# Performance work log

Measured on AMD Instinct MI355X. Metric: run time of the kernel, lower is better.

The kernel has to match this reference:

```python
import jax, jax.numpy as jnp
import numpy as np

WS = 7          # window_size (square)
HEADS = 12


def _relative_position_index(ws=WS):
    # Faithful port of WindowAttentionBase._get_relative_position_index
    coords = np.stack(np.meshgrid(np.arange(ws), np.arange(ws), indexing='ij'))  # [2, ws, ws]
    flat = coords.reshape(2, -1)                       # [2, n]
    rel = flat[:, :, None] - flat[:, None, :]          # [2, n, n]
    rel = rel.transpose(1, 2, 0)                       # [n, n, 2]
    rel[:, :, 0] += ws - 1
    rel[:, :, 1] += ws - 1
    rel[:, :, 0] *= 2 * ws - 1
    return jnp.asarray(rel.sum(-1).reshape(-1), dtype=jnp.int32)  # [n*n]


def setup_inputs() -> dict:
    key = jax.random.key(0)
    ks = jax.random.split(key, 6)
    b, H, W, c = 32, 56, 56, 384
    return {
        "x": jax.random.normal(ks[0], (b, H, W, c), jnp.float32),
        "w_qkv": jax.random.normal(ks[1], (3 * c, c), jnp.float32) * (c ** -0.5),
        "b_qkv": jax.random.normal(ks[2], (3 * c,), jnp.float32) * 0.02,
        "rel_pos": jax.random.normal(ks[3], (HEADS, (2 * WS - 1) ** 2), jnp.float32),
        "w_out": jax.random.normal(ks[4], (c, c), jnp.float32) * (c ** -0.5),
        "b_out": jax.random.normal(ks[5], (c,), jnp.float32) * 0.02,
    }


def reference(x, w_qkv, b_qkv, rel_pos, w_out, b_out):
    b, H, W, c = x.shape
    g = HEADS
    d = c // g
    hn, wn = H // WS, W // WS
    n = WS * WS
    scale = d ** -0.5

    # split_into_windows: 'b (p h) (q w) c -> b h w (p q) c'  (p,q = window dims, OUTER factors)
    xw = x.reshape(b, WS, hn, WS, wn, c).transpose(0, 2, 4, 1, 3, 5).reshape(b, hn, wn, n, c)

    qkv = xw @ w_qkv.T + b_qkv                          # [b, hn, wn, n, 3c]
    q, k, v = jnp.split(qkv, 3, axis=-1)
    # 'b h w n (g d) -> b g h w n d'
    to_heads = lambda t: t.reshape(b, hn, wn, n, g, d).transpose(0, 4, 1, 2, 3, 5)
    q, k, v = to_heads(q) * scale, to_heads(k), to_heads(v)

    sim = jnp.einsum('bghwnd,bghwmd->bghwnm', q, k)     # [b, g, hn, wn, n, n]
    idx = _relative_position_index()
    bias = rel_pos[:, idx].reshape(g, n, n)             # gather relative position bias
    sim = sim + bias[None, :, None, None, :, :]

    attn = jax.nn.softmax(sim, axis=-1)
    out = jnp.einsum('bghwnm,bghwmd->bghwnd', attn, v)  # [b, g, hn, wn, n, d]

    # 'b g h w n d -> b h w n (g d)' then merge_windows 'b h w (p q) c -> b (p h) (q w) c'
    out = out.transpose(0, 2, 3, 4, 1, 5).reshape(b, hn, wn, n, c)
    out = out.reshape(b, hn, wn, WS, WS, c).transpose(0, 3, 1, 4, 2, 5).reshape(b, H, W, c)
    return out @ w_out.T + b_out
```

## Files before the change

kernel.cpp:

```cpp
#include <hip/hip_runtime.h>

typedef __attribute__((ext_vector_type(8))) short bf16x8;
typedef __attribute__((ext_vector_type(4))) float f32x4;

__device__ __forceinline__ unsigned short f2bf(float f){
  unsigned u = __builtin_bit_cast(unsigned, f);
  u += 0x7fffu + ((u >> 16) & 1u);
  return (unsigned short)(u >> 16);
}

__device__ __forceinline__ unsigned cvt_pk_bf16(float lo, float hi){
  unsigned r;
  asm("v_cvt_pk_bf16_f32 %0, %1, %2" : "=v"(r) : "v"(lo), "v"(hi));
  return r;
}

#define ASYNC16(ldsp, gp) __builtin_amdgcn_global_load_lds( \
    (const __attribute__((address_space(1))) unsigned int*)(gp), \
    (__attribute__((address_space(3))) unsigned int*)(ldsp), 16, 0, 0)

__global__ __launch_bounds__(256) void convert_x_kernel(const float* __restrict__ x,
                                                        unsigned short* __restrict__ xb){
  int idx = blockIdx.x*256 + threadIdx.x;
  int token = idx / 96, j = idx - token*96;
  int b = token / 3136, rem = token - b*3136;
  int rr = rem / 56, cp = rem - rr*56;
  int p = rr >> 3, h = rr & 7, q = cp >> 3, w = cp & 7;
  int orow = ((b*8 + h)*8 + w)*49 + p*7 + q;
  float4 v = *(const float4*)(x + (size_t)idx*4);
  ushort4 o;
  o.x = f2bf(v.x); o.y = f2bf(v.y); o.z = f2bf(v.z); o.w = f2bf(v.w);
  *(ushort4*)(xb + (size_t)orow*384 + j*4) = o;
}

__global__ __launch_bounds__(256) void convert_w_kernel(const float* __restrict__ wq,
                                                        const float* __restrict__ wo,
                                                        unsigned short* __restrict__ wqb,
                                                        unsigned short* __restrict__ wob){
  int idx = blockIdx.x*256 + threadIdx.x;
  if (idx < 110592){
    float4 v = *(const float4*)(wq + (size_t)idx*4);
    ushort4 o; o.x=f2bf(v.x); o.y=f2bf(v.y); o.z=f2bf(v.z); o.w=f2bf(v.w);
    *(ushort4*)(wqb + (size_t)idx*4) = o;
  } else {
    int k = idx - 110592;
    float4 v = *(const float4*)(wo + (size_t)k*4);
    ushort4 o; o.x=f2bf(v.x); o.y=f2bf(v.y); o.z=f2bf(v.z); o.w=f2bf(v.w);
    *(ushort4*)(wob + (size_t)k*4) = o;
  }
}

__global__ __launch_bounds__(256) void build_btab(const float* __restrict__ rel_pos,
                                                  float* __restrict__ btab){
  int idx = blockIdx.x*256 + threadIdx.x;
  int head = idx >> 10, rem = idx & 1023;
  int fi = rem >> 6, lane = rem & 63;
  int ti = fi >> 2, tj = fi & 3;
  int qq = tj*16 + (lane & 15);
  int kb = ti*16 + (lane >> 4)*4;
  float4 v; float* vp = (float*)&v;
#pragma unroll
  for (int r=0; r<4; ++r){
    int kk = kb + r;
    float val;
    if (kk >= 49) val = -__builtin_inff();
    else if (qq >= 49) val = 0.f;
    else {
      int ip = qq/7, iq = qq - ip*7, jp = kk/7, jq = kk - jp*7;
      val = rel_pos[head*169 + (ip-jp+6)*13 + (iq-jq+6)] * 1.4426950408889634f;
    }
    vp[r] = val;
  }
  *(float4*)(btab + (size_t)idx*4) = v;
}

template<int EPI, int NBY>
__global__ __launch_bounds__(256) void gemm128(const unsigned short* __restrict__ A,
                                               const unsigned short* __restrict__ B,
                                               const float* __restrict__ bias,
                                               unsigned short* __restrict__ qo,
                                               unsigned short* __restrict__ ko,
                                               unsigned short* __restrict__ vo,
                                               float* __restrict__ out)
{
  constexpr int K = 384;
  constexpr int NT = 12;
  __shared__ unsigned short Al[3][128*32];
  __shared__ unsigned short Bl[3][128*32];
  const int tid = threadIdx.x;
  const int lane = tid & 63, wid = tid >> 6;
  const int wr = wid >> 1, wc = wid & 1;
  const int l15 = lane & 15, kg = lane >> 4;
  const int swz = (l15 >> 1) & 3;
  const int cswz = (tid & 3) ^ ((tid >> 3) & 3);

  const int n = blockIdx.x;
  const int xcd = n & 7, s = n >> 3;
  const int panel = s / NBY, nb = s - panel*NBY;
  const int bx = panel*8 + xcd, by = nb;

  const unsigned short* Ag = A + ((size_t)bx*128 + (tid>>2))*K + cswz*8;
  const unsigned short* Bg = B + ((size_t)by*128 + (tid>>2))*K + cswz*8;

  f32x4 acc[4][4] = {};

#define STAGE(buf, kt) do { \
    ASYNC16(&Al[buf][wid*512],        Ag + (kt)*32); \
    ASYNC16(&Al[buf][wid*512 + 2048], Ag + (size_t)64*K + (kt)*32); \
    ASYNC16(&Bl[buf][wid*512],        Bg + (kt)*32); \
    ASYNC16(&Bl[buf][wid*512 + 2048], Bg + (size_t)64*K + (kt)*32); \
  } while(0)

  STAGE(0,0); STAGE(1,1);

#pragma unroll
  for (int t = 0; t < NT; ++t){
    if (t < NT-1) asm volatile("s_waitcnt vmcnt(4)\n\ts_barrier" ::: "memory");
    else          asm volatile("s_waitcnt vmcnt(0)\n\ts_barrier" ::: "memory");

    if (t + 2 < NT) STAGE((t+2)%3, t+2);

    const unsigned short* Ab = Al[t % 3];
    const unsigned short* Bb = Bl[t % 3];
    bf16x8 af[4], bfv[4];
#pragma unroll
    for (int ti=0; ti<4; ++ti)
      af[ti] = *(const bf16x8*)(Ab + (wr*64 + ti*16 + l15)*32 + (kg ^ swz)*8);
#pragma unroll
    for (int tj=0; tj<4; ++tj)
      bfv[tj] = *(const bf16x8*)(Bb + (wc*64 + tj*16 + l15)*32 + (kg ^ swz)*8);

    __builtin_amdgcn_s_setprio(1);
#pragma unroll
    for (int ti=0; ti<4; ++ti)
#pragma unroll
      for (int tj=0; tj<4; ++tj)
        acc[ti][tj] = __builtin_amdgcn_mfma_f32_16x16x32_bf16(af[ti], bfv[tj], acc[ti][tj], 0,0,0);
    __builtin_amdgcn_s_setprio(0);
  }
#undef STAGE

  const int rbase = bx*128 + wr*64 + kg*4;

  if (EPI == 0){
    const int t = by / 3;
    unsigned short* __restrict__ Pout = (t==0) ? qo : ((t==1) ? ko : vo);
    const float scale = (t==0) ? (0.17677669529663689f * 1.4426950408889634f) : 1.0f;
    const int cb = (by - t*3)*128 + wc*64;
    int hoff[4]; float bvs[4];
#pragma unroll
    for (int tj=0; tj<4; ++tj){
      int colt = cb + tj*16;
      hoff[tj] = (colt>>5)*1568 + (colt&31) + l15;
      bvs[tj] = bias[by*128 + wc*64 + tj*16 + l15] * scale;
    }
#pragma unroll
    for (int ti=0; ti<4; ++ti){
#pragma unroll
      for (int r=0; r<4; ++r){
        int R = rbase + ti*16 + r;
        int win = R / 49, nn = R - win*49;
        size_t rowoff = (size_t)win*18816 + nn*32;
#pragma unroll
        for (int tj=0; tj<4; ++tj)
          Pout[rowoff + hoff[tj]] = f2bf(acc[ti][tj][r]*scale + bvs[tj]);
      }
    }
  } else {
    const int cbs = by*128 + wc*64;
    float bv[4];
#pragma unroll
    for (int tj=0; tj<4; ++tj) bv[tj] = bias[cbs + tj*16 + l15];
#pragma unroll
    for (int ti=0; ti<4; ++ti){
#pragma unroll
      for (int r=0; r<4; ++r){
        int R = rbase + ti*16 + r;
        int win = R / 49, nn = R - win*49;
        int p = nn / 7, q = nn - p*7;
        int h = (win >> 3) & 7, w = win & 7;
        size_t tok = (size_t)(win >> 6)*3136 + (size_t)((p*8 + h)*56 + q*8 + w);
        float* __restrict__ orow = out + tok*384 + cbs + l15;
#pragma unroll
        for (int tj=0; tj<4; ++tj)
          orow[tj*16] = acc[ti][tj][r] + bv[tj];
      }
    }
  }
}

__global__ __launch_bounds__(256) void attn_kernel(const unsigned short* __restrict__ q,
                                                   const unsigned short* __restrict__ k,
                                                   const unsigned short* __restrict__ v,
                                                   const float* __restrict__ btab,
                                                   unsigned short* __restrict__ ao)
{
  __shared__ unsigned short P[4][4096];
  const int tid = threadIdx.x, lane = tid & 63, wid = tid >> 6;
  const int l15 = lane & 15, kg = lane >> 4;
  const int win = blockIdx.x / 3;
  const int head = (blockIdx.x % 3)*4 + wid;
  const size_t base = ((size_t)win*12 + head)*1568;
  const unsigned short* qb = q + base;
  const unsigned short* kb = k + base;
  const unsigned short* vb = v + base;
  const float* bt = btab + head*4096;

  bf16x8 vfk[2][2];
#pragma unroll
  for (int ks=0; ks<2; ++ks)
#pragma unroll
    for (int tjv=0; tjv<2; ++tjv)
#pragma unroll
      for (int e=0; e<8; ++e)
        vfk[ks][tjv][e] = (short)vb[(ks*32 + kg*8 + e)*32 + tjv*16 + l15];

  f32x4 s[4][4];
#pragma unroll
  for (int ti=0; ti<4; ++ti)
#pragma unroll
    for (int tj=0; tj<4; ++tj)
      s[ti][tj] = *(const f32x4*)(bt + ((ti*4 + tj)*64 + lane)*4);

  bf16x8 kf[4], qf[4];
#pragma unroll
  for (int ti=0; ti<4; ++ti) kf[ti] = *(const bf16x8*)(kb + (ti*16+l15)*32 + kg*8);
#pragma unroll
  for (int tj=0; tj<4; ++tj) qf[tj] = *(const bf16x8*)(qb + (tj*16+l15)*32 + kg*8);

  __builtin_amdgcn_s_setprio(1);
#pragma unroll
  for (int ti=0; ti<4; ++ti)
#pragma unroll
    for (int tj=0; tj<4; ++tj)
      s[ti][tj] = __builtin_amdgcn_mfma_f32_16x16x32_bf16(kf[ti], qf[tj], s[ti][tj], 0,0,0);
  __builtin_amdgcn_s_setprio(0);

  float rinv[4];
#pragma unroll
  for (int tj=0; tj<4; ++tj){
    float sum = 0.f;
#pragma unroll
    for (int ti=0; ti<4; ++ti)
#pragma unroll
      for (int r=0; r<4; ++r){
        float e = exp2f(s[ti][tj][r]);
        s[ti][tj][r] = e;
        sum += e;
      }
    sum += __shfl_xor(sum, 16);
    sum += __shfl_xor(sum, 32);
    rinv[tj] = __builtin_amdgcn_rcpf(sum);
  }

  unsigned short* Pl = P[wid];
  const unsigned swz = (unsigned)((l15 & 7) << 4);
#pragma unroll
  for (int tj=0; tj<4; ++tj){
    const float rv = rinv[tj];
    const unsigned rowb = (unsigned)((tj*16 + l15)*128);
#pragma unroll
    for (int ti=0; ti<4; ++ti){
      uint2 d;
      d.x = cvt_pk_bf16(s[ti][tj][0]*rv, s[ti][tj][1]*rv);
      d.y = cvt_pk_bf16(s[ti][tj][2]*rv, s[ti][tj][3]*rv);
      unsigned boff = (rowb + (unsigned)(ti*32 + kg*8)) ^ swz;
      *(uint2*)((char*)Pl + boff) = d;
    }
  }

  f32x4 o[4][2] = {};
#pragma unroll
  for (int oti=0; oti<4; ++oti){
    bf16x8 pa[2];
#pragma unroll
    for (int ks=0; ks<2; ++ks){
      unsigned boff = ((unsigned)((oti*16+l15)*128 + ks*64 + kg*16)) ^ swz;
      pa[ks] = *(const bf16x8*)((char*)Pl + boff);
    }
    __builtin_amdgcn_s_setprio(1);
#pragma unroll
    for (int tjv=0; tjv<2; ++tjv){
      o[oti][tjv] = __builtin_amdgcn_mfma_f32_16x16x32_bf16(pa[0], vfk[0][tjv], o[oti][tjv], 0,0,0);
      o[oti][tjv] = __builtin_amdgcn_mfma_f32_16x16x32_bf16(pa[1], vfk[1][tjv], o[oti][tjv], 0,0,0);
    }
    __builtin_amdgcn_s_setprio(0);
  }

#pragma unroll
  for (int oti=0; oti<4; ++oti)
#pragma unroll
    for (int r=0; r<4; ++r){
      int row = oti*16 + kg*4 + r;
      if (row < 49){
        unsigned short* op = ao + ((size_t)win*49 + row)*384 + head*32 + l15;
        op[0]  = (unsigned short)cvt_pk_bf16(o[oti][0][r], o[oti][0][r]);
        op[16] = (unsigned short)cvt_pk_bf16(o[oti][1][r], o[oti][1][r]);
      }
    }
}

extern "C" void kernel_launch(void* const* d_in, const int* in_sizes, int n_in,
                              void* d_out, int out_size, void* d_ws, size_t ws_size,
                              hipStream_t stream)
{
  const float* x       = (const float*)d_in[0];
  const float* w_qkv   = (const float*)d_in[1];
  const float* b_qkv   = (const float*)d_in[2];
  const float* rel_pos = (const float*)d_in[3];
  const float* w_out   = (const float*)d_in[4];
  const float* b_out   = (const float*)d_in[5];
  float* out = (float*)d_out;

  char* ws = (char*)d_ws;
  unsigned short* wqb = (unsigned short*)ws;
  unsigned short* wob = (unsigned short*)(ws + 884736);
  float* btab         = (float*)(ws + 884736 + 294912);
  unsigned short* qws = (unsigned short*)(ws + 1376256);
  unsigned short* kws = qws + 38535168;
  unsigned short* vws = kws + 38535168;
  unsigned short* xb  = vws + 38535168;
  unsigned short* ao  = xb;

  convert_x_kernel<<<dim3(37632), dim3(256), 0, stream>>>(x, xb);
  convert_w_kernel<<<dim3(576),   dim3(256), 0, stream>>>(w_qkv, w_out, wqb, wob);
  build_btab<<<dim3(48), dim3(256), 0, stream>>>(rel_pos, btab);
  gemm128<0,9><<<dim3(7056), dim3(256), 0, stream>>>(xb, wqb, b_qkv, qws, kws, vws, nullptr);
  attn_kernel<<<dim3(6144), dim3(256), 0, stream>>>(qws, kws, vws, btab, ao);
  gemm128<1,3><<<dim3(2352), dim3(256), 0, stream>>>(ao, wob, b_out, nullptr, nullptr, nullptr, out);
}
```

Measured before the change: 309.6 us.

## Load GEMM B operand directly from global into registers, bypassing LDS

The weight (B) tiles in the bf16 GEMM are no longer staged through shared memory. Each wave loads its own B fragments straight from global memory into a double-buffered register array, while A stays on the triple-buffered LDS async path. This halves LDS footprint and LDS read traffic per tile, which can raise occupancy. In exchange, the two column-half waves sharing a B slice each fetch it separately, and the loads are uncoalesced row-strided 16-byte accesses. The waitcnt counts are adjusted to cover the extra outstanding register loads.

After: 403.9 us. +30.4%, slower.

```diff
diff --git a/kernel.cpp b/kernel.cpp
--- a/kernel.cpp
+++ b/kernel.cpp
@@ -86,7 +86,6 @@
   constexpr int K = 384;
   constexpr int NT = 12;
   __shared__ unsigned short Al[3][128*32];
-  __shared__ unsigned short Bl[3][128*32];
   const int tid = threadIdx.x;
   const int lane = tid & 63, wid = tid >> 6;
   const int wr = wid >> 1, wc = wid & 1;
@@ -100,45 +99,52 @@
   const int bx = panel*8 + xcd, by = nb;
 
   const unsigned short* Ag = A + ((size_t)bx*128 + (tid>>2))*K + cswz*8;
-  const unsigned short* Bg = B + ((size_t)by*128 + (tid>>2))*K + cswz*8;
+  const unsigned short* Bg0 = B + ((size_t)(by*128 + wc*64 + l15))*K + kg*8;
+  const unsigned short* Bg1 = Bg0 + (size_t)16*K;
+  const unsigned short* Bg2 = Bg0 + (size_t)32*K;
+  const unsigned short* Bg3 = Bg0 + (size_t)48*K;
 
   f32x4 acc[4][4] = {};
-
-#define STAGE(buf, kt) do { \
+  bf16x8 bfr[2][4];
+
+#define STAGE_A(buf, kt) do { \
     ASYNC16(&Al[buf][wid*512],        Ag + (kt)*32); \
     ASYNC16(&Al[buf][wid*512 + 2048], Ag + (size_t)64*K + (kt)*32); \
-    ASYNC16(&Bl[buf][wid*512],        Bg + (kt)*32); \
-    ASYNC16(&Bl[buf][wid*512 + 2048], Bg + (size_t)64*K + (kt)*32); \
   } while(0)
-
-  STAGE(0,0); STAGE(1,1);
+#define LOADB(d, kt) do { \
+    bfr[d][0] = *(const bf16x8*)(Bg0 + (kt)*32); \
+    bfr[d][1] = *(const bf16x8*)(Bg1 + (kt)*32); \
+    bfr[d][2] = *(const bf16x8*)(Bg2 + (kt)*32); \
+    bfr[d][3] = *(const bf16x8*)(Bg3 + (kt)*32); \
+  } while(0)
+
+  STAGE_A(0,0); STAGE_A(1,1);
+  LOADB(0, 0);
 
 #pragma unroll
   for (int t = 0; t < NT; ++t){
-    if (t < NT-1) asm volatile("s_waitcnt vmcnt(4)\n\ts_barrier" ::: "memory");
-    else          asm volatile("s_waitcnt vmcnt(0)\n\ts_barrier" ::: "memory");
-
-    if (t + 2 < NT) STAGE((t+2)%3, t+2);
+    if (t < NT-1) asm volatile("s_waitcnt vmcnt(6)\n\ts_barrier" ::: "memory");
+    else          asm volatile("s_waitcnt vmcnt(4)\n\ts_barrier" ::: "memory");
+
+    if (t + 2 < NT) STAGE_A((t+2)%3, t+2);
+    if (t + 1 < NT) LOADB((t+1)&1, t+1);
 
     const unsigned short* Ab = Al[t % 3];
-    const unsigned short* Bb = Bl[t % 3];
-    bf16x8 af[4], bfv[4];
+    bf16x8 af[4];
 #pragma unroll
     for (int ti=0; ti<4; ++ti)
       af[ti] = *(const bf16x8*)(Ab + (wr*64 + ti*16 + l15)*32 + (kg ^ swz)*8);
-#pragma unroll
-    for (int tj=0; tj<4; ++tj)
-      bfv[tj] = *(const bf16x8*)(Bb + (wc*64 + tj*16 + l15)*32 + (kg ^ swz)*8);
 
     __builtin_amdgcn_s_setprio(1);
 #pragma unroll
     for (int ti=0; ti<4; ++ti)
 #pragma unroll
       for (int tj=0; tj<4; ++tj)
-        acc[ti][tj] = __builtin_amdgcn_mfma_f32_16x16x32_bf16(af[ti], bfv[tj], acc[ti][tj], 0,0,0);
+        acc[ti][tj] = __builtin_amdgcn_mfma_f32_16x16x32_bf16(af[ti], bfr[t&1][tj], acc[ti][tj], 0,0,0);
     __builtin_amdgcn_s_setprio(0);
   }
-#undef STAGE
+#undef STAGE_A
+#undef LOADB
 
   const int rbase = bx*128 + wr*64 + kg*4;
 
```

## Fuse x fp32-to-bf16 window conversion into the QKV GEMM A-tile loads

Applied to the files above, without the earlier changes.

Removes the standalone convert_x kernel. The QKV GEMM now gathers fp32 x rows directly by window token index, converts them to bf16 in registers and writes them swizzled into a double-buffered LDS A tile. The weight tile keeps its async global-to-LDS path with triple buffering. This avoids a full write and re-read of the bf16 windowed copy of x, but each block now reads fp32 A data, twice the bytes, repeated across the nine N tiles, and carries more register pressure.

After: 348.7 us. +12.6%, slower.

```diff
diff --git a/kernel.cpp b/kernel.cpp
--- a/kernel.cpp
+++ b/kernel.cpp
@@ -18,20 +18,6 @@
 #define ASYNC16(ldsp, gp) __builtin_amdgcn_global_load_lds( \
     (const __attribute__((address_space(1))) unsigned int*)(gp), \
     (__attribute__((address_space(3))) unsigned int*)(ldsp), 16, 0, 0)
-
-__global__ __launch_bounds__(256) void convert_x_kernel(const float* __restrict__ x,
-                                                        unsigned short* __restrict__ xb){
-  int idx = blockIdx.x*256 + threadIdx.x;
-  int token = idx / 96, j = idx - token*96;
-  int b = token / 3136, rem = token - b*3136;
-  int rr = rem / 56, cp = rem - rr*56;
-  int p = rr >> 3, h = rr & 7, q = cp >> 3, w = cp & 7;
-  int orow = ((b*8 + h)*8 + w)*49 + p*7 + q;
-  float4 v = *(const float4*)(x + (size_t)idx*4);
-  ushort4 o;
-  o.x = f2bf(v.x); o.y = f2bf(v.y); o.z = f2bf(v.z); o.w = f2bf(v.w);
-  *(ushort4*)(xb + (size_t)orow*384 + j*4) = o;
-}
 
 __global__ __launch_bounds__(256) void convert_w_kernel(const float* __restrict__ wq,
                                                         const float* __restrict__ wo,
@@ -74,14 +60,131 @@
   *(float4*)(btab + (size_t)idx*4) = v;
 }
 
-template<int EPI, int NBY>
-__global__ __launch_bounds__(256) void gemm128(const unsigned short* __restrict__ A,
-                                               const unsigned short* __restrict__ B,
-                                               const float* __restrict__ bias,
-                                               unsigned short* __restrict__ qo,
-                                               unsigned short* __restrict__ ko,
-                                               unsigned short* __restrict__ vo,
-                                               float* __restrict__ out)
+__global__ __launch_bounds__(256) void gemm_qkv(const float* __restrict__ X,
+                                                const unsigned short* __restrict__ B,
+                                                const float* __restrict__ bias,
+                                                unsigned short* __restrict__ qo,
+                                                unsigned short* __restrict__ ko,
+                                                unsigned short* __restrict__ vo)
+{
+  constexpr int K = 384;
+  constexpr int NT = 12;
+  __shared__ unsigned short Al[2][4096];
+  __shared__ unsigned short Bl[3][4096];
+  const int tid = threadIdx.x;
+  const int lane = tid & 63, wid = tid >> 6;
+  const int wr = wid >> 1, wc = wid & 1;
+  const int l15 = lane & 15, kg = lane >> 4;
+  const int swz = (l15 >> 1) & 3;
+  const int cswz = (tid & 3) ^ ((tid >> 3) & 3);
+
+  const int n = blockIdx.x;
+  const int xcd = n & 7, s = n >> 3;
+  const int panel = s / 9, nb = s - panel*9;
+  const int bx = panel*8 + xcd, by = nb;
+
+  const int r1 = tid >> 2, c4 = tid & 3;
+  int R1 = bx*128 + r1, R2 = R1 + 64;
+  int win1 = R1/49, nn1 = R1 - win1*49, p1 = nn1/7, q1 = nn1 - p1*7;
+  int win2 = R2/49, nn2 = R2 - win2*49, p2 = nn2/7, q2 = nn2 - p2*7;
+  size_t tok1 = (size_t)(win1>>6)*3136 + (p1*8 + ((win1>>3)&7))*56 + q1*8 + (win1&7);
+  size_t tok2 = (size_t)(win2>>6)*3136 + (p2*8 + ((win2>>3)&7))*56 + q2*8 + (win2&7);
+  const float* Xg1 = X + tok1*384 + c4*8;
+  const float* Xg2 = X + tok2*384 + c4*8;
+  const int wch = (c4 ^ ((r1 >> 1) & 3)) * 8;
+  unsigned short* Aw1base = &Al[0][0] + r1*32 + wch;
+  unsigned short* Aw2base = Aw1base + 64*32;
+
+  const unsigned short* Bg = B + ((size_t)(by*128 + (tid>>2)))*K + cswz*8;
+
+  f32x4 acc[4][4] = {};
+  float4 aA0[2], aA1[2], aB0[2], aB1[2];
+
+#define LOADA(st, kt) do { \
+    aA0[st] = *(const float4*)(Xg1 + (kt)*32); \
+    aA1[st] = *(const float4*)(Xg1 + (kt)*32 + 4); \
+    aB0[st] = *(const float4*)(Xg2 + (kt)*32); \
+    aB1[st] = *(const float4*)(Xg2 + (kt)*32 + 4); \
+  } while(0)
+#define WRITEA(st, buf) do { \
+    uint4 u1, u2; \
+    u1.x = cvt_pk_bf16(aA0[st].x, aA0[st].y); u1.y = cvt_pk_bf16(aA0[st].z, aA0[st].w); \
+    u1.z = cvt_pk_bf16(aA1[st].x, aA1[st].y); u1.w = cvt_pk_bf16(aA1[st].z, aA1[st].w); \
+    u2.x = cvt_pk_bf16(aB0[st].x, aB0[st].y); u2.y = cvt_pk_bf16(aB0[st].z, aB0[st].w); \
+    u2.z = cvt_pk_bf16(aB1[st].x, aB1[st].y); u2.w = cvt_pk_bf16(aB1[st].z, aB1[st].w); \
+    *(uint4*)(Aw1base + (buf)*4096) = u1; \
+    *(uint4*)(Aw2base + (buf)*4096) = u2; \
+  } while(0)
+#define STAGE_B(buf, kt) do { \
+    ASYNC16(&Bl[buf][wid*512],        Bg + (kt)*32); \
+    ASYNC16(&Bl[buf][wid*512 + 2048], Bg + (size_t)64*K + (kt)*32); \
+  } while(0)
+
+  LOADA(0, 0); STAGE_B(0, 0);
+  LOADA(1, 1); STAGE_B(1, 1);
+  asm volatile("s_waitcnt vmcnt(8)" ::: "memory");
+  WRITEA(0, 0);
+
+#pragma unroll
+  for (int t = 0; t < NT; ++t){
+    if (t < NT-1) asm volatile("s_waitcnt vmcnt(6) lgkmcnt(0)\n\ts_barrier" ::: "memory");
+    else          asm volatile("s_waitcnt vmcnt(0) lgkmcnt(0)\n\ts_barrier" ::: "memory");
+
+    if (t < NT-1) WRITEA((t+1)&1, (t+1)&1);
+    if (t < NT-2){ LOADA(t&1, t+2); STAGE_B((t+2)%3, t+2); }
+
+    const unsigned short* Ab = Al[t & 1];
+    const unsigned short* Bb = Bl[t % 3];
+    bf16x8 af[4], bfv[4];
+#pragma unroll
+    for (int ti=0; ti<4; ++ti)
+      af[ti] = *(const bf16x8*)(Ab + (wr*64 + ti*16 + l15)*32 + (kg ^ swz)*8);
+#pragma unroll
+    for (int tj=0; tj<4; ++tj)
+      bfv[tj] = *(const bf16x8*)(Bb + (wc*64 + tj*16 + l15)*32 + (kg ^ swz)*8);
+
+    __builtin_amdgcn_s_setprio(1);
+#pragma unroll
+    for (int ti=0; ti<4; ++ti)
+#pragma unroll
+      for (int tj=0; tj<4; ++tj)
+        acc[ti][tj] = __builtin_amdgcn_mfma_f32_16x16x32_bf16(af[ti], bfv[tj], acc[ti][tj], 0,0,0);
+    __builtin_amdgcn_s_setprio(0);
+  }
+#undef LOADA
+#undef WRITEA
+#undef STAGE_B
+
+  const int rbase = bx*128 + wr*64 + kg*4;
+  const int t = by / 3;
+  unsigned short* __restrict__ Pout = (t==0) ? qo : ((t==1) ? ko : vo);
+  const float scale = (t==0) ? (0.17677669529663689f * 1.4426950408889634f) : 1.0f;
+  const int cb = (by - t*3)*128 + wc*64;
+  int hoff[4]; float bvs[4];
+#pragma unroll
+  for (int tj=0; tj<4; ++tj){
+    int colt = cb + tj*16;
+    hoff[tj] = (colt>>5)*1568 + (colt&31) + l15;
+    bvs[tj] = bias[by*128 + wc*64 + tj*16 + l15] * scale;
+  }
+#pragma unroll
+  for (int ti=0; ti<4; ++ti){
+#pragma unroll
+    for (int r=0; r<4; ++r){
+      int R = rbase + ti*16 + r;
+      int win = R / 49, nn = R - win*49;
+      size_t rowoff = (size_t)win*18816 + nn*32;
+#pragma unroll
+      for (int tj=0; tj<4; ++tj)
+        Pout[rowoff + hoff[tj]] = f2bf(acc[ti][tj][r]*scale + bvs[tj]);
+    }
+  }
+}
+
+__global__ __launch_bounds__(256) void gemm_out(const unsigned short* __restrict__ A,
+                                                const unsigned short* __restrict__ B,
+                                                const float* __restrict__ bias,
+                                                float* __restrict__ out)
 {
   constexpr int K = 384;
   constexpr int NT = 12;
@@ -96,11 +199,11 @@
 
   const int n = blockIdx.x;
   const int xcd = n & 7, s = n >> 3;
-  const int panel = s / NBY, nb = s - panel*NBY;
+  const int panel = s / 3, nb = s - panel*3;
   const int bx = panel*8 + xcd, by = nb;
 
   const unsigned short* Ag = A + ((size_t)bx*128 + (tid>>2))*K + cswz*8;
-  const unsigned short* Bg = B + ((size_t)by*128 + (tid>>2))*K + cswz*8;
+  const unsigned short* Bg = B + ((size_t)(by*128 + (tid>>2)))*K + cswz*8;
 
   f32x4 acc[4][4] = {};
 
@@ -141,50 +244,23 @@
 #undef STAGE
 
   const int rbase = bx*128 + wr*64 + kg*4;
-
-  if (EPI == 0){
-    const int t = by / 3;
-    unsigned short* __restrict__ Pout = (t==0) ? qo : ((t==1) ? ko : vo);
-    const float scale = (t==0) ? (0.17677669529663689f * 1.4426950408889634f) : 1.0f;
-    const int cb = (by - t*3)*128 + wc*64;
-    int hoff[4]; float bvs[4];
-#pragma unroll
-    for (int tj=0; tj<4; ++tj){
-      int colt = cb + tj*16;
-      hoff[tj] = (colt>>5)*1568 + (colt&31) + l15;
-      bvs[tj] = bias[by*128 + wc*64 + tj*16 + l15] * scale;
-    }
-#pragma unroll
-    for (int ti=0; ti<4; ++ti){
-#pragma unroll
-      for (int r=0; r<4; ++r){
-        int R = rbase + ti*16 + r;
-        int win = R / 49, nn = R - win*49;
-        size_t rowoff = (size_t)win*18816 + nn*32;
-#pragma unroll
-        for (int tj=0; tj<4; ++tj)
-          Pout[rowoff + hoff[tj]] = f2bf(acc[ti][tj][r]*scale + bvs[tj]);
-      }
-    }
-  } else {
-    const int cbs = by*128 + wc*64;
-    float bv[4];
-#pragma unroll
-    for (int tj=0; tj<4; ++tj) bv[tj] = bias[cbs + tj*16 + l15];
-#pragma unroll
-    for (int ti=0; ti<4; ++ti){
-#pragma unroll
-      for (int r=0; r<4; ++r){
-        int R = rbase + ti*16 + r;
-        int win = R / 49, nn = R - win*49;
-        int p = nn / 7, q = nn - p*7;
-        int h = (win >> 3) & 7, w = win & 7;
-        size_t tok = (size_t)(win >> 6)*3136 + (size_t)((p*8 + h)*56 + q*8 + w);
-        float* __restrict__ orow = out + tok*384 + cbs + l15;
-#pragma unroll
-        for (int tj=0; tj<4; ++tj)
-          orow[tj*16] = acc[ti][tj][r] + bv[tj];
-      }
+  const int cbs = by*128 + wc*64;
+  float bv[4];
+#pragma unroll
+  for (int tj=0; tj<4; ++tj) bv[tj] = bias[cbs + tj*16 + l15];
+#pragma unroll
+  for (int ti=0; ti<4; ++ti){
+#pragma unroll
+    for (int r=0; r<4; ++r){
+      int R = rbase + ti*16 + r;
+      int win = R / 49, nn = R - win*49;
+      int p = nn / 7, q = nn - p*7;
+      int h = (win >> 3) & 7, w = win & 7;
+      size_t tok = (size_t)(win >> 6)*3136 + (size_t)((p*8 + h)*56 + q*8 + w);
+      float* __restrict__ orow = out + tok*384 + cbs + l15;
+#pragma unroll
+      for (int tj=0; tj<4; ++tj)
+        orow[tj*16] = acc[ti][tj][r] + bv[tj];
     }
   }
 }
@@ -319,13 +395,11 @@
   unsigned short* qws = (unsigned short*)(ws + 1376256);
   unsigned short* kws = qws + 38535168;
   unsigned short* vws = kws + 38535168;
-  unsigned short* xb  = vws + 38535168;
-  unsigned short* ao  = xb;
-
-  convert_x_kernel<<<dim3(37632), dim3(256), 0, stream>>>(x, xb);
-  convert_w_kernel<<<dim3(576),   dim3(256), 0, stream>>>(w_qkv, w_out, wqb, wob);
+  unsigned short* ao  = vws + 38535168;
+
+  convert_w_kernel<<<dim3(576), dim3(256), 0, stream>>>(w_qkv, w_out, wqb, wob);
   build_btab<<<dim3(48), dim3(256), 0, stream>>>(rel_pos, btab);
-  gemm128<0,9><<<dim3(7056), dim3(256), 0, stream>>>(xb, wqb, b_qkv, qws, kws, vws, nullptr);
+  gemm_qkv<<<dim3(7056), dim3(256), 0, stream>>>(x, wqb, b_qkv, qws, kws, vws);
   attn_kernel<<<dim3(6144), dim3(256), 0, stream>>>(qws, kws, vws, btab, ao);
-  gemm128<1,3><<<dim3(2352), dim3(256), 0, stream>>>(ao, wob, b_out, nullptr, nullptr, nullptr, out);
-}
+  gemm_out<<<dim3(2352), dim3(256), 0, stream>>>(ao, wob, b_out, out);
+}
```

## Restructure GEMM to 256x128 tiles with 8 waves and interleaved staging

Applied to the files above, without the earlier changes.

Replaces the 128x128, 4-wave GEMM with a 256x128 tile run by 512 threads (8 waves), K-step 64 and an XOR-swizzled LDS layout. The async global-to-LDS loads for the next stage are split into two halves and interleaved with two MFMA phases, separated by barriers, so fewer but larger blocks are launched. The aim is more operand reuse per LDS load and better overlap of memory traffic with MFMA work. In exchange LDS use rises to about 144 KB per block and each iteration adds extra barriers, which may limit occupancy.

Result: slower. 326.8 us (+5.5%).

```diff
diff --git a/kernel.cpp b/kernel.cpp
--- a/kernel.cpp
+++ b/kernel.cpp
@@ -75,72 +75,113 @@
 }
 
 template<int EPI, int NBY>
-__global__ __launch_bounds__(256) void gemm128(const unsigned short* __restrict__ A,
-                                               const unsigned short* __restrict__ B,
-                                               const float* __restrict__ bias,
-                                               unsigned short* __restrict__ qo,
-                                               unsigned short* __restrict__ ko,
-                                               unsigned short* __restrict__ vo,
-                                               float* __restrict__ out)
+__global__ __launch_bounds__(512) void gemm8p(const unsigned short* __restrict__ A,
+                                              const unsigned short* __restrict__ B,
+                                              const float* __restrict__ bias,
+                                              unsigned short* __restrict__ qo,
+                                              unsigned short* __restrict__ ko,
+                                              unsigned short* __restrict__ vo,
+                                              float* __restrict__ out)
 {
   constexpr int K = 384;
-  constexpr int NT = 12;
-  __shared__ unsigned short Al[3][128*32];
-  __shared__ unsigned short Bl[3][128*32];
+  __shared__ unsigned short Al[3][256*64];
+  __shared__ unsigned short Bl[3][128*64];
   const int tid = threadIdx.x;
   const int lane = tid & 63, wid = tid >> 6;
   const int wr = wid >> 1, wc = wid & 1;
   const int l15 = lane & 15, kg = lane >> 4;
-  const int swz = (l15 >> 1) & 3;
-  const int cswz = (tid & 3) ^ ((tid >> 3) & 3);
+  const int xr = l15 & 7;
 
   const int n = blockIdx.x;
   const int xcd = n & 7, s = n >> 3;
   const int panel = s / NBY, nb = s - panel*NBY;
   const int bx = panel*8 + xcd, by = nb;
 
-  const unsigned short* Ag = A + ((size_t)bx*128 + (tid>>2))*K + cswz*8;
-  const unsigned short* Bg = B + ((size_t)by*128 + (tid>>2))*K + cswz*8;
+  const int srow = wid*8 + (lane>>3);
+  const int schunk = (lane & 7) ^ (lane >> 3);
+  const unsigned short* AgS = A + ((size_t)(bx*256 + srow))*K + schunk*8;
+  const unsigned short* BgS = B + ((size_t)(by*128 + srow))*K + schunk*8;
+
+#define STAGE_A(buf, kt, ss) ASYNC16(&Al[buf][(ss)*4096 + wid*512], AgS + (size_t)(ss)*64*K + (kt)*64)
+#define STAGE_B(buf, kt, ss) ASYNC16(&Bl[buf][(ss)*4096 + wid*512], BgS + (size_t)(ss)*64*K + (kt)*64)
+
+  int offA[4][2], offB[4][2];
+#pragma unroll
+  for (int ti=0; ti<4; ++ti){
+    int rowA = wr*64 + ti*16 + l15;
+    int rowB = wc*64 + ti*16 + l15;
+#pragma unroll
+    for (int ks=0; ks<2; ++ks){
+      offA[ti][ks] = rowA*64 + (((ks*4 + kg) ^ xr)*8);
+      offB[ti][ks] = rowB*64 + (((ks*4 + kg) ^ xr)*8);
+    }
+  }
 
   f32x4 acc[4][4] = {};
 
-#define STAGE(buf, kt) do { \
-    ASYNC16(&Al[buf][wid*512],        Ag + (kt)*32); \
-    ASYNC16(&Al[buf][wid*512 + 2048], Ag + (size_t)64*K + (kt)*32); \
-    ASYNC16(&Bl[buf][wid*512],        Bg + (kt)*32); \
-    ASYNC16(&Bl[buf][wid*512 + 2048], Bg + (size_t)64*K + (kt)*32); \
-  } while(0)
-
-  STAGE(0,0); STAGE(1,1);
-
-#pragma unroll
-  for (int t = 0; t < NT; ++t){
-    if (t < NT-1) asm volatile("s_waitcnt vmcnt(4)\n\ts_barrier" ::: "memory");
-    else          asm volatile("s_waitcnt vmcnt(0)\n\ts_barrier" ::: "memory");
-
-    if (t + 2 < NT) STAGE((t+2)%3, t+2);
-
-    const unsigned short* Ab = Al[t % 3];
-    const unsigned short* Bb = Bl[t % 3];
-    bf16x8 af[4], bfv[4];
-#pragma unroll
-    for (int ti=0; ti<4; ++ti)
-      af[ti] = *(const bf16x8*)(Ab + (wr*64 + ti*16 + l15)*32 + (kg ^ swz)*8);
+  STAGE_A(0,0,0); STAGE_A(0,0,1); STAGE_A(0,0,2); STAGE_A(0,0,3);
+  STAGE_B(0,0,0); STAGE_B(0,0,1);
+  STAGE_A(1,1,0); STAGE_A(1,1,1); STAGE_A(1,1,2); STAGE_A(1,1,3);
+  STAGE_B(1,1,0); STAGE_B(1,1,1);
+  asm volatile("s_waitcnt vmcnt(6)\n\ts_barrier" ::: "memory");
+
+#pragma unroll
+  for (int t = 0; t < 6; ++t){
+    const int buf = t % 3, nbuf = (t + 2) % 3;
+    const unsigned short* Ab = Al[buf];
+    const unsigned short* Bb = Bl[buf];
+
+    bf16x8 af01[2][2], bfv[4][2];
+#pragma unroll
+    for (int ti=0; ti<2; ++ti)
+#pragma unroll
+      for (int ks=0; ks<2; ++ks)
+        af01[ti][ks] = *(const bf16x8*)(Ab + offA[ti][ks]);
 #pragma unroll
     for (int tj=0; tj<4; ++tj)
-      bfv[tj] = *(const bf16x8*)(Bb + (wc*64 + tj*16 + l15)*32 + (kg ^ swz)*8);
+#pragma unroll
+      for (int ks=0; ks<2; ++ks)
+        bfv[tj][ks] = *(const bf16x8*)(Bb + offB[tj][ks]);
+    if (t < 4){ STAGE_A(nbuf, t+2, 0); STAGE_A(nbuf, t+2, 1); STAGE_A(nbuf, t+2, 2); }
+    asm volatile("s_barrier" ::: "memory");
 
     __builtin_amdgcn_s_setprio(1);
 #pragma unroll
-    for (int ti=0; ti<4; ++ti)
-#pragma unroll
-      for (int tj=0; tj<4; ++tj)
-        acc[ti][tj] = __builtin_amdgcn_mfma_f32_16x16x32_bf16(af[ti], bfv[tj], acc[ti][tj], 0,0,0);
+    for (int ti=0; ti<2; ++ti)
+#pragma unroll
+      for (int tj=0; tj<4; ++tj){
+        acc[ti][tj] = __builtin_amdgcn_mfma_f32_16x16x32_bf16(af01[ti][0], bfv[tj][0], acc[ti][tj], 0,0,0);
+        acc[ti][tj] = __builtin_amdgcn_mfma_f32_16x16x32_bf16(af01[ti][1], bfv[tj][1], acc[ti][tj], 0,0,0);
+      }
     __builtin_amdgcn_s_setprio(0);
-  }
-#undef STAGE
-
-  const int rbase = bx*128 + wr*64 + kg*4;
+    asm volatile("s_barrier" ::: "memory");
+
+    bf16x8 af23[2][2];
+#pragma unroll
+    for (int ti=0; ti<2; ++ti)
+#pragma unroll
+      for (int ks=0; ks<2; ++ks)
+        af23[ti][ks] = *(const bf16x8*)(Ab + offA[2+ti][ks]);
+    if (t < 4){ STAGE_A(nbuf, t+2, 3); STAGE_B(nbuf, t+2, 0); STAGE_B(nbuf, t+2, 1); }
+    asm volatile("s_barrier" ::: "memory");
+
+    __builtin_amdgcn_s_setprio(1);
+#pragma unroll
+    for (int ti=0; ti<2; ++ti)
+#pragma unroll
+      for (int tj=0; tj<4; ++tj){
+        acc[2+ti][tj] = __builtin_amdgcn_mfma_f32_16x16x32_bf16(af23[ti][0], bfv[tj][0], acc[2+ti][tj], 0,0,0);
+        acc[2+ti][tj] = __builtin_amdgcn_mfma_f32_16x16x32_bf16(af23[ti][1], bfv[tj][1], acc[2+ti][tj], 0,0,0);
+      }
+    __builtin_amdgcn_s_setprio(0);
+
+    if (t < 4)       asm volatile("s_waitcnt vmcnt(6)\n\ts_barrier" ::: "memory");
+    else if (t == 4) asm volatile("s_waitcnt vmcnt(0)\n\ts_barrier" ::: "memory");
+  }
+#undef STAGE_A
+#undef STAGE_B
+
+  const int rbase = bx*256 + wr*64 + kg*4;
 
   if (EPI == 0){
     const int t = by / 3;
@@ -325,7 +366,7 @@
   convert_x_kernel<<<dim3(37632), dim3(256), 0, stream>>>(x, xb);
   convert_w_kernel<<<dim3(576),   dim3(256), 0, stream>>>(w_qkv, w_out, wqb, wob);
   build_btab<<<dim3(48), dim3(256), 0, stream>>>(rel_pos, btab);
-  gemm128<0,9><<<dim3(7056), dim3(256), 0, stream>>>(xb, wqb, b_qkv, qws, kws, vws, nullptr);
+  gemm8p<0,9><<<dim3(3528), dim3(512), 0, stream>>>(xb, wqb, b_qkv, qws, kws, vws, nullptr);
   attn_kernel<<<dim3(6144), dim3(256), 0, stream>>>(qws, kws, vws, btab, ao);
-  gemm128<1,3><<<dim3(2352), dim3(256), 0, stream>>>(ao, wob, b_out, nullptr, nullptr, nullptr, out);
-}
+  gemm8p<1,3><<<dim3(1176), dim3(512), 0, stream>>>(ao, wob, b_out, nullptr, nullptr, nullptr, out);
+}
```
